# Kernel optimization log

Measured on AMD Instinct MI355X. Metric: run time of the kernel, lower is better.

## Reference

```python
import jax, jax.numpy as jnp
import numpy as np

TEMP = 0.07
EPS = 1e-8
NUM_CLASSES = 7
THRESH = 0.3


def setup_inputs() -> dict:
    key = jax.random.key(0)
    k1, k2, k3, k4, k5 = jax.random.split(key, 5)
    N, H, E, C = 8192, 128, 256, NUM_CLASSES
    reps = jax.random.normal(k1, (N, H), dtype=jnp.float32)
    labels = jax.random.randint(k2, (N,), 0, C, dtype=jnp.int64 if jax.config.jax_enable_x64 else jnp.int32)
    centers = jax.random.normal(k3, (C, E), dtype=jnp.float32)
    fc_w = jax.random.normal(k4, (H, E), dtype=jnp.float32) * (1.0 / np.sqrt(E))
    fc_b = jax.random.normal(k5, (H,), dtype=jnp.float32) * 0.01
    return {"reps": reps, "labels": labels, "centers": centers, "fc_w": fc_w, "fc_b": fc_b}


def reference(reps, labels, centers, fc_w, fc_b):
    # fc(default_centers): [C, H]
    curr_centers = centers @ fc_w.T + fc_b
    pad_labels = jnp.arange(NUM_CLASSES, dtype=labels.dtype)

    all_reps = jnp.concatenate([reps, curr_centers], axis=0)      # [M, H]
    all_labels = jnp.concatenate([labels, pad_labels], axis=0)    # [M]
    B = reps.shape[0]
    M = all_reps.shape[0]

    # cosine similarity via normalized matmul (avoids [B,M,H] broadcast)
    norms = jnp.sqrt(jnp.sum(all_reps * all_reps, axis=-1))
    rn = all_reps / jnp.maximum(norms, 1e-8)[:, None]
    cos = rn[:B] @ rn.T                                           # [B, M]

    scores = (1.0 + cos) * 0.5 + EPS
    eye = (jnp.arange(B)[:, None] == jnp.arange(M)[None, :]).astype(scores.dtype)
    scores = scores * (1.0 - eye) / TEMP
    # torch uses .item() on the max -> a non-differentiable constant
    scores = scores - jax.lax.stop_gradient(jnp.max(scores))
    e = jnp.exp(scores)

    pos_mask = (labels[:, None] == all_labels[None, :]).astype(scores.dtype)  # [B, M]
    mask = 1.0 - eye

    pos_sum = jnp.sum(e * pos_mask * mask, axis=-1)
    neg_sum = jnp.sum(e * (1.0 - pos_mask), axis=-1)
    probs = pos_sum / (pos_sum + neg_sum)
    probs = probs / (jnp.sum(pos_mask * mask, axis=-1) + EPS)

    loss_vec = -jnp.log(probs + EPS)
    loss_mask = (loss_vec > THRESH).astype(loss_vec.dtype)
    denom = jax.lax.stop_gradient(jnp.sum(loss_mask)) + EPS
    loss = jnp.sum(loss_vec * loss_mask) / denom
    return loss
```

## Files before the change

kernel.cpp:

```cpp
#include <hip/hip_runtime.h>
#include <hip/hip_bf16.h>

#define BN 8192
#define MM 8199
#define MP 8208
#define HH 128
#define EE 256
#define JCHUNKS 64
#define GX 128
#define GY 16
#define NUM_HIST 7

typedef __attribute__((ext_vector_type(8))) short short8;
typedef __attribute__((ext_vector_type(4))) float floatx4;

__global__ __launch_bounds__(256)
void prep_kernel(const float* __restrict__ reps,
                 const int* __restrict__ labels,
                 const float* __restrict__ centers,
                 const float* __restrict__ fc_w,
                 const float* __restrict__ fc_b,
                 __hip_bfloat16* __restrict__ rn,
                 int* __restrict__ labp,
                 float* __restrict__ tot) {
  const int wid = threadIdx.x >> 6, lane = threadIdx.x & 63;
  const int b = blockIdx.x;
  if (b < 2048) {
    if (threadIdx.x < 8) tot[b * 8 + threadIdx.x] = 0.f;
    const int r = b * 4 + wid;
    float2 v = ((const float2*)(reps + (size_t)r * HH))[lane];
    float ss = v.x * v.x + v.y * v.y;
#pragma unroll
    for (int m = 1; m < 64; m <<= 1) ss += __shfl_xor(ss, m);
    float inv = 1.0f / fmaxf(sqrtf(ss), 1e-8f);
    __hip_bfloat162 h2;
    h2.x = __float2bfloat16(v.x * inv);
    h2.y = __float2bfloat16(v.y * inv);
    ((__hip_bfloat162*)(rn + (size_t)r * HH))[lane] = h2;
    if (lane == 0) labp[r] = labels[r];
  } else {
    __shared__ float currs[7 * HH];
    for (int o = threadIdx.x; o < 7 * HH; o += 256) {
      int c = o >> 7, h = o & 127;
      const float4* ce = (const float4*)(centers + c * EE);
      const float4* w  = (const float4*)(fc_w + h * EE);
      float s = 0.f;
#pragma unroll 4
      for (int j = 0; j < EE / 4; ++j) {
        float4 a = ce[j], bb = w[j];
        s += a.x * bb.x + a.y * bb.y + a.z * bb.z + a.w * bb.w;
      }
      currs[o] = s + fc_b[h];
    }
    __syncthreads();
    for (int k = 0; k < 4; ++k) {
      int c = wid * 4 + k;
      int r = BN + c;
      float2 v = make_float2(0.f, 0.f);
      if (c < 7) v = ((const float2*)(currs + c * HH))[lane];
      float ss = v.x * v.x + v.y * v.y;
#pragma unroll
      for (int m = 1; m < 64; m <<= 1) ss += __shfl_xor(ss, m);
      float inv = 1.0f / fmaxf(sqrtf(ss), 1e-8f);
      __hip_bfloat162 h2;
      h2.x = __float2bfloat16(v.x * inv);
      h2.y = __float2bfloat16(v.y * inv);
      ((__hip_bfloat162*)(rn + (size_t)r * HH))[lane] = h2;
      if (lane == 0) labp[r] = (r < MM) ? r - BN : -1;
    }
  }
}

__global__ __launch_bounds__(256, 2)
void main_kernel(const __hip_bfloat16* __restrict__ rn,
                 const int* __restrict__ labp,
                 float* __restrict__ tot,
                 float* __restrict__ pos) {
  __shared__ float red[128];
  const int lane = threadIdx.x & 63;
  const int wid  = threadIdx.x >> 6;
  const int q = lane >> 4, col = lane & 15;
  const int ibase = blockIdx.x * 64;
  const int chunk = (blockIdx.y << 2) | wid;
  const short* rns = (const short*)rn;

  if (threadIdx.x < 128) red[threadIdx.x] = 0.f;

  short8 afrag[4][4];
#pragma unroll
  for (int it = 0; it < 4; ++it) {
    const short8* p = (const short8*)(rns + (size_t)(ibase + it * 16 + col) * HH + q * 8);
    afrag[it][0] = p[0];
    afrag[it][1] = p[4];
    afrag[it][2] = p[8];
    afrag[it][3] = p[12];
  }
  int labi[4][4];
#pragma unroll
  for (int it = 0; it < 4; ++it)
#pragma unroll
    for (int r = 0; r < 4; ++r)
      labi[it][r] = labp[ibase + it * 16 + q * 4 + r];

  float stot[4][4] = {};
  float spos[4][4] = {};
  const float K2 = 10.30496147f;

  const short* bptr = rns + (size_t)(chunk * 16 + col) * HH + q * 8;
  const int* lptr = labp + chunk * 16 + col;

  for (int jb = chunk * 16; jb < MP; jb += 16 * JCHUNKS) {
    short8 b0 = ((const short8*)bptr)[0];
    short8 b1 = ((const short8*)bptr)[4];
    short8 b2 = ((const short8*)bptr)[8];
    short8 b3 = ((const short8*)bptr)[12];
    const int labj = *lptr;
    bptr += 16 * JCHUNKS * HH;
    lptr += 16 * JCHUNKS;
#pragma unroll
    for (int it = 0; it < 4; ++it) {
      floatx4 acc = {0.f, 0.f, 0.f, 0.f};
      acc = __builtin_amdgcn_mfma_f32_16x16x32_bf16(afrag[it][0], b0, acc, 0, 0, 0);
      acc = __builtin_amdgcn_mfma_f32_16x16x32_bf16(afrag[it][1], b1, acc, 0, 0, 0);
      acc = __builtin_amdgcn_mfma_f32_16x16x32_bf16(afrag[it][2], b2, acc, 0, 0, 0);
      acc = __builtin_amdgcn_mfma_f32_16x16x32_bf16(afrag[it][3], b3, acc, 0, 0, 0);
      const bool isdiag = (jb == ibase + it * 16);
#pragma unroll
      for (int r = 0; r < 4; ++r) {
        float e = __builtin_amdgcn_exp2f(fmaf(acc[r], K2, -K2));
        if (isdiag && (col == q * 4 + r)) e = 0.f;
        float m = (labj == labi[it][r]) ? 1.0f : 0.0f;
        stot[it][r] += e;
        spos[it][r] = fmaf(m, e, spos[it][r]);
      }
    }
  }

  __syncthreads();

#pragma unroll
  for (int it = 0; it < 4; ++it)
#pragma unroll
    for (int r = 0; r < 4; ++r) {
      float tt = stot[it][r], pp = spos[it][r];
#pragma unroll
      for (int m = 1; m <= 8; m <<= 1) {
        tt += __shfl_xor(tt, m);
        pp += __shfl_xor(pp, m);
      }
      if (col == 0) {
        int li = it * 16 + q * 4 + r;
        atomicAdd(&red[li], tt);
        atomicAdd(&red[64 + li], pp);
      }
    }
  __syncthreads();
  if (threadIdx.x < 64)       atomicAdd(&tot[ibase + threadIdx.x], red[threadIdx.x]);
  else if (threadIdx.x < 128) atomicAdd(&pos[ibase + threadIdx.x - 64], red[threadIdx.x]);
}

__global__ __launch_bounds__(1024)
void loss_kernel(const float* __restrict__ tot,
                 const float* __restrict__ pos,
                 const int* __restrict__ labels,
                 float* __restrict__ out) {
  __shared__ int hist[NUM_HIST];
  __shared__ float s1[16], s2[16];
  const int tid = threadIdx.x;
  const int lane = tid & 63, wid = tid >> 6;
  if (tid < NUM_HIST) hist[tid] = 0;
  __syncthreads();
  int c0 = 0, c1 = 0, c2 = 0, c3 = 0, c4 = 0, c5 = 0, c6 = 0;
  for (int i = tid; i < BN; i += 1024) {
    int lab = labels[i];
    unsigned long long m0 = __ballot(lab == 0);
    unsigned long long m1 = __ballot(lab == 1);
    unsigned long long m2 = __ballot(lab == 2);
    unsigned long long m3 = __ballot(lab == 3);
    unsigned long long m4 = __ballot(lab == 4);
    unsigned long long m5 = __ballot(lab == 5);
    unsigned long long m6 = __ballot(lab == 6);
    if (lane == 0) {
      c0 += __popcll(m0); c1 += __popcll(m1); c2 += __popcll(m2);
      c3 += __popcll(m3); c4 += __popcll(m4); c5 += __popcll(m5);
      c6 += __popcll(m6);
    }
  }
  if (lane == 0) {
    atomicAdd(&hist[0], c0); atomicAdd(&hist[1], c1); atomicAdd(&hist[2], c2);
    atomicAdd(&hist[3], c3); atomicAdd(&hist[4], c4); atomicAdd(&hist[5], c5);
    atomicAdd(&hist[6], c6);
  }
  __syncthreads();
  const float K2 = 10.30496147f;
  const float epad9 = 9.0f * exp2f(-K2);
  float lsum = 0.f, msum = 0.f;
  for (int i = tid; i < BN; i += 1024) {
    float t = tot[i] - epad9;
    float p = pos[i];
    float c = (float)hist[labels[i]];
    float pr = (p / t) / (c + 1e-8f);
    float lv = -logf(pr + 1e-8f);
    if (lv > 0.3f) { lsum += lv; msum += 1.f; }
  }
#pragma unroll
  for (int m = 1; m < 64; m <<= 1) {
    lsum += __shfl_xor(lsum, m);
    msum += __shfl_xor(msum, m);
  }
  if (lane == 0) { s1[wid] = lsum; s2[wid] = msum; }
  __syncthreads();
  if (wid == 0) {
    float a = (lane < 16) ? s1[lane] : 0.f;
    float b = (lane < 16) ? s2[lane] : 0.f;
#pragma unroll
    for (int m = 1; m < 16; m <<= 1) {
      a += __shfl_xor(a, m);
      b += __shfl_xor(b, m);
    }
    if (lane == 0) out[0] = a / (b + 1e-8f);
  }
}

extern "C" void kernel_launch(void* const* d_in, const int* in_sizes, int n_in,
                              void* d_out, int out_size, void* d_ws, size_t ws_size,
                              hipStream_t stream) {
  const float* reps    = (const float*)d_in[0];
  const int*   labels  = (const int*)d_in[1];
  const float* centers = (const float*)d_in[2];
  const float* fc_w    = (const float*)d_in[3];
  const float* fc_b    = (const float*)d_in[4];
  float* out = (float*)d_out;

  char* ws = (char*)d_ws;
  int* labp   = (int*)(ws + 4096);
  __hip_bfloat16* rn = (__hip_bfloat16*)(ws + 40960);
  float* tot = (float*)(ws + 40960 + 2101248);
  float* pos = tot + BN;

  prep_kernel<<<2049, 256, 0, stream>>>(reps, labels, centers, fc_w, fc_b, rn, labp, tot);
  main_kernel<<<dim3(GX, GY), 256, 0, stream>>>(rn, labp, tot, pos);
  loss_kernel<<<1, 1024, 0, stream>>>(tot, pos, labels, out);
}
```

Before: 162.3 us.

## Assign contiguous column ranges per wave and double-buffer B fragment loads

Each wave now handles a contiguous block of 128 columns instead of striding across the matrix with a 64-chunk interleave. The loop is fully unrolled over 8 tiles, and B fragments for the next pair of tiles are prefetched into a second register buffer while the current pair is computed. The tail tile of padded center rows is handled separately by the last chunk. This is meant to hide global load latency behind MFMA and exp work, at the cost of more VGPRs, which may pressure occupancy under the launch bound of 2.

```diff
diff --git a/kernel.cpp b/kernel.cpp
--- a/kernel.cpp
+++ b/kernel.cpp
@@ -6,7 +6,6 @@
 #define MP 8208
 #define HH 128
 #define EE 256
-#define JCHUNKS 64
 #define GX 128
 #define GY 16
 #define NUM_HIST 7
@@ -82,6 +81,7 @@
   const int q = lane >> 4, col = lane & 15;
   const int ibase = blockIdx.x * 64;
   const int chunk = (blockIdx.y << 2) | wid;
+  const int jrow0 = chunk * 128;
   const short* rns = (const short*)rn;
 
   if (threadIdx.x < 128) red[threadIdx.x] = 0.f;
@@ -102,38 +102,66 @@
     for (int r = 0; r < 4; ++r)
       labi[it][r] = labp[ibase + it * 16 + q * 4 + r];
 
+  int labj[8];
+#pragma unroll
+  for (int t = 0; t < 8; ++t) labj[t] = labp[jrow0 + t * 16 + col];
+
   float stot[4][4] = {};
   float spos[4][4] = {};
   const float K2 = 10.30496147f;
 
-  const short* bptr = rns + (size_t)(chunk * 16 + col) * HH + q * 8;
-  const int* lptr = labp + chunk * 16 + col;
-
-  for (int jb = chunk * 16; jb < MP; jb += 16 * JCHUNKS) {
-    short8 b0 = ((const short8*)bptr)[0];
-    short8 b1 = ((const short8*)bptr)[4];
-    short8 b2 = ((const short8*)bptr)[8];
-    short8 b3 = ((const short8*)bptr)[12];
-    const int labj = *lptr;
-    bptr += 16 * JCHUNKS * HH;
-    lptr += 16 * JCHUNKS;
+  const short* jbase = rns + (size_t)(jrow0 + col) * HH + q * 8;
+
+  auto compute_tile = [&](const short8* bfr, int labjv, int jb) {
 #pragma unroll
     for (int it = 0; it < 4; ++it) {
       floatx4 acc = {0.f, 0.f, 0.f, 0.f};
-      acc = __builtin_amdgcn_mfma_f32_16x16x32_bf16(afrag[it][0], b0, acc, 0, 0, 0);
-      acc = __builtin_amdgcn_mfma_f32_16x16x32_bf16(afrag[it][1], b1, acc, 0, 0, 0);
-      acc = __builtin_amdgcn_mfma_f32_16x16x32_bf16(afrag[it][2], b2, acc, 0, 0, 0);
-      acc = __builtin_amdgcn_mfma_f32_16x16x32_bf16(afrag[it][3], b3, acc, 0, 0, 0);
+      acc = __builtin_amdgcn_mfma_f32_16x16x32_bf16(afrag[it][0], bfr[0], acc, 0, 0, 0);
+      acc = __builtin_amdgcn_mfma_f32_16x16x32_bf16(afrag[it][1], bfr[1], acc, 0, 0, 0);
+      acc = __builtin_amdgcn_mfma_f32_16x16x32_bf16(afrag[it][2], bfr[2], acc, 0, 0, 0);
+      acc = __builtin_amdgcn_mfma_f32_16x16x32_bf16(afrag[it][3], bfr[3], acc, 0, 0, 0);
       const bool isdiag = (jb == ibase + it * 16);
 #pragma unroll
       for (int r = 0; r < 4; ++r) {
         float e = __builtin_amdgcn_exp2f(fmaf(acc[r], K2, -K2));
         if (isdiag && (col == q * 4 + r)) e = 0.f;
-        float m = (labj == labi[it][r]) ? 1.0f : 0.0f;
         stot[it][r] += e;
-        spos[it][r] = fmaf(m, e, spos[it][r]);
-      }
-    }
+        spos[it][r] += (labjv == labi[it][r]) ? e : 0.f;
+      }
+    }
+  };
+
+  short8 bufA[2][4], bufB[2][4];
+#pragma unroll
+  for (int u = 0; u < 2; ++u) {
+    const short8* p = (const short8*)(jbase + (size_t)(u * 16) * HH);
+    bufA[u][0] = p[0]; bufA[u][1] = p[4]; bufA[u][2] = p[8]; bufA[u][3] = p[12];
+  }
+
+#pragma unroll
+  for (int pr = 0; pr < 4; ++pr) {
+    short8 (*cur)[4] = (pr & 1) ? bufB : bufA;
+    short8 (*nxt)[4] = (pr & 1) ? bufA : bufB;
+    if (pr < 3) {
+#pragma unroll
+      for (int u = 0; u < 2; ++u) {
+        const short8* p = (const short8*)(jbase + (size_t)((pr * 2 + 2 + u) * 16) * HH);
+        nxt[u][0] = p[0]; nxt[u][1] = p[4]; nxt[u][2] = p[8]; nxt[u][3] = p[12];
+      }
+    }
+#pragma unroll
+    for (int u = 0; u < 2; ++u) {
+      const int t = pr * 2 + u;
+      compute_tile(cur[u], labj[t], jrow0 + t * 16);
+    }
+  }
+
+  if (chunk == 63) {
+    const short8* p = (const short8*)(rns + (size_t)(8192 + col) * HH + q * 8);
+    short8 tb[4];
+    tb[0] = p[0]; tb[1] = p[4]; tb[2] = p[8]; tb[3] = p[12];
+    int lj = labp[8192 + col];
+    compute_tile(tb, lj, 8192);
   }
 
   __syncthreads();
```

Measured after the change: 170.8 us. 1.05x slower.
